# Kernel tuning notes

Measured on AMD Instinct MI355X. Metric: run time of the kernel, lower is better.

## Reference

```python
import jax, jax.numpy as jnp
import numpy as np

NEG_INF = -1e30


def _rope_interleaved(x, freqs):
    # x: [B,S,H,D], freqs broadcastable [1,S,1,D]; interleaved even/odd rotation
    x0 = x[..., 0::2]
    x1 = x[..., 1::2]
    f0 = freqs[..., 0::2]
    f1 = freqs[..., 1::2]
    o0 = f0 * x0 - f1 * x1
    o1 = f1 * x0 + f0 * x1
    # interleave back: out[...,0::2]=o0, out[...,1::2]=o1
    out = jnp.stack([o0, o1], axis=-1)  # [B,S,H,D/2,2]
    return out.reshape(x.shape).astype(x.dtype)


def setup_inputs() -> dict:
    key = jax.random.key(0)
    kq, kk, kv, kf = jax.random.split(key, 4)
    B, S, H, D = 2, 2048, 16, 128
    q = jax.random.normal(kq, (B, S, H, D), dtype=jnp.float32)
    k = jax.random.normal(kk, (B, S, H, D), dtype=jnp.float32)
    v = jax.random.normal(kv, (B, S, H, D), dtype=jnp.float32)
    freqs = jax.random.normal(kf, (1, S, 1, D), dtype=jnp.float32)
    return {"q": q, "k": k, "v": v, "freqs": freqs}


def reference(q, k, v, freqs):
    # RoPE (Wan-style indexed interleaved write) on q and k
    rq = _rope_interleaved(q, freqs)  # [B,S,H,D]
    rk = _rope_interleaved(k, freqs)
    B, S, H, D = q.shape
    scale = 1.0 / jnp.sqrt(jnp.asarray(D, dtype=q.dtype))
    # transpose(1,2) -> [B,H,S,D]; fused into einsum subscripts
    scores = jnp.einsum("bqhd,bkhd->bhqk", rq, rk) * scale  # [B,H,S,S]
    causal = jnp.tril(jnp.ones((S, S), dtype=bool))
    scores = jnp.where(causal[None, None, :, :], scores, NEG_INF)
    probs = jax.nn.softmax(scores, axis=-1)
    out = jnp.einsum("bhqk,bkhd->bhqd", probs, v)  # [B,H,S,D]
    return out
```

## Files before the change

kernel.cpp:

```cpp
#include <hip/hip_runtime.h>
#include <hip/hip_bf16.h>

#define B_  2
#define S_  2048
#define H_  16
#define D_  128
#define BQ  128
#define BK  64
#define SH  (H_ * D_)
#define NT  (S_ / 64)
#define NTQ (S_ / BQ)
#define TILE_US 8192

typedef __attribute__((ext_vector_type(8))) short bf16x8;
typedef __attribute__((ext_vector_type(4))) float f32x4;
typedef __attribute__((ext_vector_type(4))) unsigned int u32x4;

__device__ __forceinline__ ushort f2bf(float x) {
  union { float f; unsigned u; } c; c.f = x;
  unsigned u = c.u;
  return (ushort)((u + 0x7FFFu + ((u >> 16) & 1u)) >> 16);
}

__device__ __forceinline__ void gload_lds16(const ushort* g, ushort* l) {
  __builtin_amdgcn_global_load_lds((const __attribute__((address_space(1))) void*)g,
                                   (__attribute__((address_space(3))) void*)l,
                                   16, 0, 0);
}

__device__ __forceinline__ bf16x8 ntload8(const ushort* p) {
  union { u32x4 u; bf16x8 v; } c;
  c.u = __builtin_nontemporal_load((const u32x4*)p);
  return c.v;
}

__device__ __forceinline__ unsigned cvt_pk_bf16(float lo, float hi) {
  unsigned d;
  asm("v_cvt_pk_bf16_f32 %0, %1, %2" : "=v"(d) : "v"(lo), "v"(hi));
  return d;
}

__global__ __launch_bounds__(256)
void pack_all(const float* __restrict__ qg, const float* __restrict__ kg,
              const float* __restrict__ vg, const float* __restrict__ fg,
              ushort* __restrict__ qr, ushort* __restrict__ kr,
              ushort* __restrict__ vt) {
  __shared__ float sv[64][133];
  const int bhp = blockIdx.x;
  const int t   = blockIdx.y;
  const int b   = bhp >> 4;
  const int h   = bhp & 15;
  const int tid = threadIdx.x;
  const float QS = 0.08838834764831845f * 1.4426950408889634f;
  const size_t tbase = ((size_t)(b * H_ + h) * NT + t) * TILE_US;

  #pragma unroll
  for (int c = 0; c < 4; c++) {
    const int idx = tid + 256 * c;
    const int row = idx >> 4;
    const int cu  = idx & 15;
    const int col = cu * 8;
    const int s   = t * 64 + row;
    const size_t goff = ((size_t)(b * S_ + s)) * SH + (size_t)h * D_ + col;

    const float4 f0 = *(const float4*)(fg + (size_t)s * D_ + col);
    const float4 f1 = *(const float4*)(fg + (size_t)s * D_ + col + 4);
    const float4 qx0 = *(const float4*)(qg + goff);
    const float4 qx1 = *(const float4*)(qg + goff + 4);
    const float4 kx0 = *(const float4*)(kg + goff);
    const float4 kx1 = *(const float4*)(kg + goff + 4);
    const float4 vx0 = *(const float4*)(vg + goff);
    const float4 vx1 = *(const float4*)(vg + goff + 4);

    *(float4*)&sv[row][col]     = vx0;
    *(float4*)&sv[row][col + 4] = vx1;

    union { ushort s[8]; uint4 v; } pq, pk;
    pq.s[0] = f2bf((f0.x*qx0.x - f0.y*qx0.y) * QS);
    pq.s[1] = f2bf((f0.y*qx0.x + f0.x*qx0.y) * QS);
    pq.s[2] = f2bf((f0.z*qx0.z - f0.w*qx0.w) * QS);
    pq.s[3] = f2bf((f0.w*qx0.z + f0.z*qx0.w) * QS);
    pq.s[4] = f2bf((f1.x*qx1.x - f1.y*qx1.y) * QS);
    pq.s[5] = f2bf((f1.y*qx1.x + f1.x*qx1.y) * QS);
    pq.s[6] = f2bf((f1.z*qx1.z - f1.w*qx1.w) * QS);
    pq.s[7] = f2bf((f1.w*qx1.z + f1.z*qx1.w) * QS);
    pk.s[0] = f2bf(f0.x*kx0.x - f0.y*kx0.y);
    pk.s[1] = f2bf(f0.y*kx0.x + f0.x*kx0.y);
    pk.s[2] = f2bf(f0.z*kx0.z - f0.w*kx0.w);
    pk.s[3] = f2bf(f0.w*kx0.z + f0.z*kx0.w);
    pk.s[4] = f2bf(f1.x*kx1.x - f1.y*kx1.y);
    pk.s[5] = f2bf(f1.y*kx1.x + f1.x*kx1.y);
    pk.s[6] = f2bf(f1.z*kx1.z - f1.w*kx1.w);
    pk.s[7] = f2bf(f1.w*kx1.z + f1.z*kx1.w);

    const int pos = ((cu >> 2) * 4 + (row >> 4)) * 64 + ((row & 15) | ((cu & 3) << 4));
    *(uint4*)(qr + tbase + (size_t)pos * 8) = pq.v;
    *(uint4*)(kr + tbase + (size_t)pos * 8) = pk.v;
  }
  __syncthreads();

  #pragma unroll
  for (int c = 0; c < 4; c++) {
    const int u2  = tid + 256 * c;
    const int g2  = u2 >> 6;
    const int ln  = u2 & 63;
    const int dim = (g2 & 7) * 16 + (ln & 15);
    const int ks2 = g2 >> 3;
    const int qd  = ln >> 4;
    union { ushort s[8]; uint4 v; } p;
    #pragma unroll
    for (int j = 0; j < 8; j++) {
      const int key = ks2 * 32 + (j >> 2) * 16 + qd * 4 + (j & 3);
      p.s[j] = f2bf(sv[key][dim]);
    }
    *(uint4*)(vt + tbase + (size_t)u2 * 8) = p.v;
  }
}

__global__ __launch_bounds__(256, 2)
void fattn4(const ushort* __restrict__ qr, const ushort* __restrict__ kr,
            const ushort* __restrict__ vt, float* __restrict__ og) {
  __shared__ __align__(16) ushort sK[2][TILE_US];
  __shared__ __align__(16) ushort sV[2][TILE_US];

  const int bh_  = blockIdx.x;
  const int qt   = NTQ - 1 - (int)blockIdx.y;
  const int tid  = threadIdx.x;
  const int wv   = tid >> 6;
  const int lane = tid & 63;
  const int l15  = lane & 15;
  const int quad = lane >> 4;

  const size_t bh = (size_t)bh_;
  const ushort* ktb = kr + bh * NT * TILE_US;
  const ushort* vtb = vt + bh * NT * TILE_US;

  bf16x8 afq[2][4];
  {
    const ushort* qtb64 = qr + (bh * NT + 2 * qt + (wv >> 1)) * TILE_US;
    const int rbb = (wv & 1) * 2;
    #pragma unroll
    for (int rh = 0; rh < 2; rh++)
      #pragma unroll
      for (int ks = 0; ks < 4; ks++)
        afq[rh][ks] = ntload8(qtb64 + (size_t)((ks * 4 + rbb + rh) * 64 + lane) * 8);
  }

  float rs[2] = {0.0f, 0.0f};
  f32x4 o_acc[2][8];
  #pragma unroll
  for (int rh = 0; rh < 2; rh++)
    #pragma unroll
    for (int dt = 0; dt < 8; dt++) o_acc[rh][dt] = (f32x4)0.0f;

  #pragma unroll
  for (int c = 0; c < 4; c++) {
    const int g = wv * 4 + c;
    gload_lds16(ktb + g * 512 + lane * 8, &sK[0][g * 512 + lane * 8]);
    gload_lds16(vtb + g * 512 + lane * 8, &sV[0][g * 512 + lane * 8]);
  }

  const int rowmax = qt * BQ + wv * 32 + 31;
  const int nkt = 2 * qt + 2;
  int buf = 0;
  for (int kt = 0; kt < nkt; kt++) {
    __syncthreads();

    if (kt + 1 < nkt) {
      const ushort* ksrc = ktb + (size_t)(kt + 1) * TILE_US;
      const ushort* vsrc = vtb + (size_t)(kt + 1) * TILE_US;
      #pragma unroll
      for (int c = 0; c < 4; c++) {
        const int g = wv * 4 + c;
        gload_lds16(ksrc + g * 512 + lane * 8, &sK[buf ^ 1][g * 512 + lane * 8]);
        gload_lds16(vsrc + g * 512 + lane * 8, &sV[buf ^ 1][g * 512 + lane * 8]);
      }
    }

    if (kt * 64 <= rowmax) {
      f32x4 sc[2][4];
      #pragma unroll
      for (int rh = 0; rh < 2; rh++)
        #pragma unroll
        for (int nt = 0; nt < 4; nt++) sc[rh][nt] = (f32x4)0.0f;
      #pragma unroll
      for (int nt = 0; nt < 4; nt++) {
        #pragma unroll
        for (int ks = 0; ks < 4; ks++) {
          const bf16x8 bk_ = *(const bf16x8*)&sK[buf][(size_t)((ks * 4 + nt) * 64 + lane) * 8];
          sc[0][nt] = __builtin_amdgcn_mfma_f32_16x16x32_bf16(bk_, afq[0][ks], sc[0][nt], 0, 0, 0);
          sc[1][nt] = __builtin_amdgcn_mfma_f32_16x16x32_bf16(bk_, afq[1][ks], sc[1][nt], 0, 0, 0);
        }
      }

      if (kt >= 2 * qt) {
        #pragma unroll
        for (int rh = 0; rh < 2; rh++) {
          const int qg = qt * 128 + wv * 32 + rh * 16 + l15;
          #pragma unroll
          for (int nt = 0; nt < 4; nt++) {
            const int kg = kt * 64 + nt * 16 + quad * 4;
            #pragma unroll
            for (int r = 0; r < 4; r++)
              if (kg + r > qg) sc[rh][nt][r] = -1e30f;
          }
        }
      }

      bf16x8 ap[2][2];
      #pragma unroll
      for (int rh = 0; rh < 2; rh++) {
        float p[4][4];
        #pragma unroll
        for (int nt = 0; nt < 4; nt++)
          #pragma unroll
          for (int r = 0; r < 4; r++) {
            p[nt][r] = __builtin_amdgcn_exp2f(sc[rh][nt][r]);
            rs[rh] += p[nt][r];
          }
        #pragma unroll
        for (int ks = 0; ks < 2; ks++) {
          union { unsigned u[4]; bf16x8 v; } pk_;
          #pragma unroll
          for (int m = 0; m < 4; m++) {
            const int nt = ks * 2 + (m >> 1);
            pk_.u[m] = cvt_pk_bf16(p[nt][2 * (m & 1)], p[nt][2 * (m & 1) + 1]);
          }
          ap[rh][ks] = pk_.v;
        }
      }

      #pragma unroll
      for (int dt = 0; dt < 8; dt++) {
        #pragma unroll
        for (int ks = 0; ks < 2; ks++) {
          const bf16x8 bv = *(const bf16x8*)&sV[buf][(size_t)((ks * 8 + dt) * 64 + lane) * 8];
          o_acc[0][dt] = __builtin_amdgcn_mfma_f32_16x16x32_bf16(ap[0][ks], bv, o_acc[0][dt], 0, 0, 0);
          o_acc[1][dt] = __builtin_amdgcn_mfma_f32_16x16x32_bf16(ap[1][ks], bv, o_acc[1][dt], 0, 0, 0);
        }
      }
    }

    buf ^= 1;
  }

  float* ob = og + (bh * S_ + (size_t)qt * BQ) * D_;
  #pragma unroll
  for (int rh = 0; rh < 2; rh++) {
    float t = rs[rh];
    t += __shfl_xor(t, 16);
    t += __shfl_xor(t, 32);
    #pragma unroll
    for (int r = 0; r < 4; r++) {
      const float inv = 1.0f / __shfl(t, quad * 4 + r);
      const int row = wv * 32 + rh * 16 + quad * 4 + r;
      #pragma unroll
      for (int dt = 0; dt < 8; dt++)
        __builtin_nontemporal_store(o_acc[rh][dt][r] * inv,
                                    &ob[(size_t)row * D_ + dt * 16 + l15]);
    }
  }
}

extern "C" void kernel_launch(void* const* d_in, const int* in_sizes, int n_in,
                              void* d_out, int out_size, void* d_ws, size_t ws_size,
                              hipStream_t stream) {
  const float* q = (const float*)d_in[0];
  const float* k = (const float*)d_in[1];
  const float* v = (const float*)d_in[2];
  const float* f = (const float*)d_in[3];
  float* o = (float*)d_out;

  const size_t NELT = (size_t)B_ * S_ * H_ * D_;
  ushort* qr = (ushort*)d_ws;
  ushort* kr = qr + NELT;
  ushort* vt = kr + NELT;

  dim3 block(256);
  pack_all<<<dim3(B_ * H_, NT), block, 0, stream>>>(q, k, v, f, qr, kr, vt);
  fattn4<<<dim3(B_ * H_, NTQ), block, 0, stream>>>(qr, kr, vt, o);
}
```

Before: 196.6 us.

## Shrink attention blocks to 64 queries, 2 waves, and load V directly from global

Replaces the 4-wave, 128-query attention block with a 2-wave, 64-query block, which doubles the grid and removes the wasted half-masked diagonal tiles. V is no longer staged through LDS. Each wave reads its V fragments straight from global memory (cached) into registers, and LDS holds only double-buffered K. This adds more parallel blocks and lowers LDS use, but each K/V tile is now reused by half as many query rows. V global loads are also exposed in the loop without prefetch.

After: 208.1 us. 1.06x slower.

```diff
diff --git a/kernel.cpp b/kernel.cpp
--- a/kernel.cpp
+++ b/kernel.cpp
@@ -5,11 +5,9 @@
 #define S_  2048
 #define H_  16
 #define D_  128
-#define BQ  128
-#define BK  64
 #define SH  (H_ * D_)
 #define NT  (S_ / 64)
-#define NTQ (S_ / BQ)
+#define NQ2 (S_ / 64)
 #define TILE_US 8192
 
 typedef __attribute__((ext_vector_type(8))) short bf16x8;
@@ -117,14 +115,13 @@
   }
 }
 
-__global__ __launch_bounds__(256, 2)
-void fattn4(const ushort* __restrict__ qr, const ushort* __restrict__ kr,
+__global__ __launch_bounds__(128, 2)
+void fattn2(const ushort* __restrict__ qr, const ushort* __restrict__ kr,
             const ushort* __restrict__ vt, float* __restrict__ og) {
   __shared__ __align__(16) ushort sK[2][TILE_US];
-  __shared__ __align__(16) ushort sV[2][TILE_US];
 
   const int bh_  = blockIdx.x;
-  const int qt   = NTQ - 1 - (int)blockIdx.y;
+  const int qt   = NQ2 - 1 - (int)blockIdx.y;
   const int tid  = threadIdx.x;
   const int wv   = tid >> 6;
   const int lane = tid & 63;
@@ -137,13 +134,12 @@
 
   bf16x8 afq[2][4];
   {
-    const ushort* qtb64 = qr + (bh * NT + 2 * qt + (wv >> 1)) * TILE_US;
-    const int rbb = (wv & 1) * 2;
+    const ushort* qtb64 = qr + (bh * NT + qt) * TILE_US;
     #pragma unroll
     for (int rh = 0; rh < 2; rh++)
       #pragma unroll
       for (int ks = 0; ks < 4; ks++)
-        afq[rh][ks] = ntload8(qtb64 + (size_t)((ks * 4 + rbb + rh) * 64 + lane) * 8);
+        afq[rh][ks] = ntload8(qtb64 + (size_t)((ks * 4 + wv * 2 + rh) * 64 + lane) * 8);
   }
 
   float rs[2] = {0.0f, 0.0f};
@@ -154,97 +150,98 @@
     for (int dt = 0; dt < 8; dt++) o_acc[rh][dt] = (f32x4)0.0f;
 
   #pragma unroll
-  for (int c = 0; c < 4; c++) {
-    const int g = wv * 4 + c;
+  for (int c = 0; c < 8; c++) {
+    const int g = wv * 8 + c;
     gload_lds16(ktb + g * 512 + lane * 8, &sK[0][g * 512 + lane * 8]);
-    gload_lds16(vtb + g * 512 + lane * 8, &sV[0][g * 512 + lane * 8]);
-  }
-
-  const int rowmax = qt * BQ + wv * 32 + 31;
-  const int nkt = 2 * qt + 2;
+  }
+
+  const int nkt = qt + 1;
   int buf = 0;
   for (int kt = 0; kt < nkt; kt++) {
     __syncthreads();
 
     if (kt + 1 < nkt) {
       const ushort* ksrc = ktb + (size_t)(kt + 1) * TILE_US;
-      const ushort* vsrc = vtb + (size_t)(kt + 1) * TILE_US;
-      #pragma unroll
-      for (int c = 0; c < 4; c++) {
-        const int g = wv * 4 + c;
+      #pragma unroll
+      for (int c = 0; c < 8; c++) {
+        const int g = wv * 8 + c;
         gload_lds16(ksrc + g * 512 + lane * 8, &sK[buf ^ 1][g * 512 + lane * 8]);
-        gload_lds16(vsrc + g * 512 + lane * 8, &sV[buf ^ 1][g * 512 + lane * 8]);
-      }
-    }
-
-    if (kt * 64 <= rowmax) {
-      f32x4 sc[2][4];
-      #pragma unroll
-      for (int rh = 0; rh < 2; rh++)
+      }
+    }
+
+    f32x4 sc[2][4];
+    #pragma unroll
+    for (int rh = 0; rh < 2; rh++)
+      #pragma unroll
+      for (int nt = 0; nt < 4; nt++) sc[rh][nt] = (f32x4)0.0f;
+    #pragma unroll
+    for (int nt = 0; nt < 4; nt++) {
+      #pragma unroll
+      for (int ks = 0; ks < 4; ks++) {
+        const bf16x8 bk_ = *(const bf16x8*)&sK[buf][(size_t)((ks * 4 + nt) * 64 + lane) * 8];
+        sc[0][nt] = __builtin_amdgcn_mfma_f32_16x16x32_bf16(bk_, afq[0][ks], sc[0][nt], 0, 0, 0);
+        sc[1][nt] = __builtin_amdgcn_mfma_f32_16x16x32_bf16(bk_, afq[1][ks], sc[1][nt], 0, 0, 0);
+      }
+    }
+
+    const ushort* vsrc = vtb + (size_t)kt * TILE_US;
+    bf16x8 bvv[2][8];
+    #pragma unroll
+    for (int ks = 0; ks < 2; ks++)
+      #pragma unroll
+      for (int dt = 0; dt < 8; dt++)
+        bvv[ks][dt] = *(const bf16x8*)(vsrc + (size_t)((ks * 8 + dt) * 64 + lane) * 8);
+
+    if (kt == qt) {
+      #pragma unroll
+      for (int rh = 0; rh < 2; rh++) {
+        const int qg = qt * 64 + wv * 32 + rh * 16 + l15;
         #pragma unroll
-        for (int nt = 0; nt < 4; nt++) sc[rh][nt] = (f32x4)0.0f;
-      #pragma unroll
-      for (int nt = 0; nt < 4; nt++) {
+        for (int nt = 0; nt < 4; nt++) {
+          const int kg = kt * 64 + nt * 16 + quad * 4;
+          #pragma unroll
+          for (int r = 0; r < 4; r++)
+            if (kg + r > qg) sc[rh][nt][r] = -1e30f;
+        }
+      }
+    }
+
+    bf16x8 ap[2][2];
+    #pragma unroll
+    for (int rh = 0; rh < 2; rh++) {
+      float p[4][4];
+      #pragma unroll
+      for (int nt = 0; nt < 4; nt++)
         #pragma unroll
-        for (int ks = 0; ks < 4; ks++) {
-          const bf16x8 bk_ = *(const bf16x8*)&sK[buf][(size_t)((ks * 4 + nt) * 64 + lane) * 8];
-          sc[0][nt] = __builtin_amdgcn_mfma_f32_16x16x32_bf16(bk_, afq[0][ks], sc[0][nt], 0, 0, 0);
-          sc[1][nt] = __builtin_amdgcn_mfma_f32_16x16x32_bf16(bk_, afq[1][ks], sc[1][nt], 0, 0, 0);
+        for (int r = 0; r < 4; r++) {
+          p[nt][r] = __builtin_amdgcn_exp2f(sc[rh][nt][r]);
+          rs[rh] += p[nt][r];
         }
-      }
-
-      if (kt >= 2 * qt) {
+      #pragma unroll
+      for (int ks = 0; ks < 2; ks++) {
+        union { unsigned u[4]; bf16x8 v; } pk_;
         #pragma unroll
-        for (int rh = 0; rh < 2; rh++) {
-          const int qg = qt * 128 + wv * 32 + rh * 16 + l15;
-          #pragma unroll
-          for (int nt = 0; nt < 4; nt++) {
-            const int kg = kt * 64 + nt * 16 + quad * 4;
-            #pragma unroll
-            for (int r = 0; r < 4; r++)
-              if (kg + r > qg) sc[rh][nt][r] = -1e30f;
-          }
+        for (int m = 0; m < 4; m++) {
+          const int nt = ks * 2 + (m >> 1);
+          pk_.u[m] = cvt_pk_bf16(p[nt][2 * (m & 1)], p[nt][2 * (m & 1) + 1]);
         }
-      }
-
-      bf16x8 ap[2][2];
-      #pragma unroll
-      for (int rh = 0; rh < 2; rh++) {
-        float p[4][4];
-        #pragma unroll
-        for (int nt = 0; nt < 4; nt++)
-          #pragma unroll
-          for (int r = 0; r < 4; r++) {
-            p[nt][r] = __builtin_amdgcn_exp2f(sc[rh][nt][r]);
-            rs[rh] += p[nt][r];
-          }
-        #pragma unroll
-        for (int ks = 0; ks < 2; ks++) {
-          union { unsigned u[4]; bf16x8 v; } pk_;
-          #pragma unroll
-          for (int m = 0; m < 4; m++) {
-            const int nt = ks * 2 + (m >> 1);
-            pk_.u[m] = cvt_pk_bf16(p[nt][2 * (m & 1)], p[nt][2 * (m & 1) + 1]);
-          }
-          ap[rh][ks] = pk_.v;
-        }
-      }
-
-      #pragma unroll
-      for (int dt = 0; dt < 8; dt++) {
-        #pragma unroll
-        for (int ks = 0; ks < 2; ks++) {
-          const bf16x8 bv = *(const bf16x8*)&sV[buf][(size_t)((ks * 8 + dt) * 64 + lane) * 8];
-          o_acc[0][dt] = __builtin_amdgcn_mfma_f32_16x16x32_bf16(ap[0][ks], bv, o_acc[0][dt], 0, 0, 0);
-          o_acc[1][dt] = __builtin_amdgcn_mfma_f32_16x16x32_bf16(ap[1][ks], bv, o_acc[1][dt], 0, 0, 0);
-        }
+        ap[rh][ks] = pk_.v;
+      }
+    }
+
+    #pragma unroll
+    for (int dt = 0; dt < 8; dt++) {
+      #pragma unroll
+      for (int ks = 0; ks < 2; ks++) {
+        o_acc[0][dt] = __builtin_amdgcn_mfma_f32_16x16x32_bf16(ap[0][ks], bvv[ks][dt], o_acc[0][dt], 0, 0, 0);
+        o_acc[1][dt] = __builtin_amdgcn_mfma_f32_16x16x32_bf16(ap[1][ks], bvv[ks][dt], o_acc[1][dt], 0, 0, 0);
       }
     }
 
     buf ^= 1;
   }
 
-  float* ob = og + (bh * S_ + (size_t)qt * BQ) * D_;
+  float* ob = og + (bh * S_ + (size_t)qt * 64) * D_;
   #pragma unroll
   for (int rh = 0; rh < 2; rh++) {
     float t = rs[rh];
@@ -276,7 +273,6 @@
   ushort* kr = qr + NELT;
   ushort* vt = kr + NELT;
 
-  dim3 block(256);
-  pack_all<<<dim3(B_ * H_, NT), block, 0, stream>>>(q, k, v, f, qr, kr, vt);
-  fattn4<<<dim3(B_ * H_, NTQ), block, 0, stream>>>(qr, kr, vt, o);
-}
+  pack_all<<<dim3(B_ * H_, NT), dim3(256), 0, stream>>>(q, k, v, f, qr, kr, vt);
+  fattn2<<<dim3(B_ * H_, NQ2), dim3(128), 0, stream>>>(qr, kr, vt, o);
+}
```
